# Kernel tuning notes

Hardware: AMD Instinct MI355X
Metric: run time of the kernel (lower is better)

The kernel has to match this reference:

```python
import jax, jax.numpy as jnp
import numpy as np

G = 160          # voxel grid extent per axis
N = 300000       # active voxels
CIN, COUT = 64, 128
EPS = 1e-4       # BatchNorm eps from module (0.0001)


def _neighbor_table(pos):
    """pos: [N,3] int32 in [0,G). Returns idx [27,N] int32, -1 where no neighbor voxel exists."""
    n = pos.shape[0]
    flat = (pos[:, 0] * G + pos[:, 1]) * G + pos[:, 2]
    grid = jnp.full((G * G * G,), -1, dtype=jnp.int32).at[flat].set(
        jnp.arange(n, dtype=jnp.int32))
    offs = jnp.array([[dx, dy, dz] for dx in (-1, 0, 1)
                      for dy in (-1, 0, 1) for dz in (-1, 0, 1)], dtype=jnp.int32)
    npos = pos[None, :, :] + offs[:, None, :]              # [27,N,3]
    inb = jnp.all((npos >= 0) & (npos < G), axis=-1)       # [27,N]
    nflat = (npos[..., 0] * G + npos[..., 1]) * G + npos[..., 2]
    nflat = jnp.where(inb, nflat, 0)
    return jnp.where(inb, grid[nflat], -1)                 # [27,N]


def _sparse_conv(feat, nbr_idx, W):
    """Submanifold sparse 3x3x3 conv. feat [N,Cin], nbr_idx [27,N], W [27,Cin,Cout]."""
    n = feat.shape[0]
    acc0 = jnp.zeros((n, W.shape[-1]), dtype=feat.dtype)

    def body(acc, xs):
        idx, Wk = xs                                       # [N], [Cin,Cout]
        valid = (idx >= 0)
        g = feat[jnp.maximum(idx, 0)] * valid[:, None].astype(feat.dtype)
        return acc + g @ Wk, None

    out, _ = jax.lax.scan(body, acc0, (nbr_idx, W))
    return out


def _bn(x, gamma, beta, mean, var):
    # eval-mode BatchNorm1d: (x - mean) / sqrt(var + eps) * gamma + beta
    return (x - mean) * jax.lax.rsqrt(var + EPS) * gamma + beta


def setup_inputs() -> dict:
    key = jax.random.key(0)
    ks = jax.random.split(key, 8)
    rng = np.random.default_rng(0)
    flat = rng.choice(G * G * G, size=N, replace=False)
    pos = np.stack(np.unravel_index(flat, (G, G, G)), axis=-1).astype(np.int32)

    feat = jax.random.normal(ks[0], (N, CIN), dtype=jnp.float32)
    lin_w = jax.random.normal(ks[1], (COUT, CIN), dtype=jnp.float32) / np.sqrt(CIN)
    W1 = jax.random.normal(ks[2], (27, CIN, COUT), dtype=jnp.float32) / np.sqrt(27 * CIN)
    W2 = jax.random.normal(ks[3], (27, COUT, COUT), dtype=jnp.float32) / np.sqrt(27 * COUT)
    return {
        "feat": feat,
        "pos": jnp.asarray(pos),
        "lin_w": lin_w,
        "bn1_gamma": jnp.ones((CIN,), jnp.float32),
        "bn1_beta": jnp.zeros((CIN,), jnp.float32),
        "bn1_mean": 0.1 * jax.random.normal(ks[4], (CIN,), dtype=jnp.float32),
        "bn1_var": 0.5 + jax.random.uniform(ks[5], (CIN,), dtype=jnp.float32),
        "W1": W1,
        "bn2_gamma": jnp.ones((COUT,), jnp.float32),
        "bn2_beta": jnp.zeros((COUT,), jnp.float32),
        "bn2_mean": 0.1 * jax.random.normal(ks[6], (COUT,), dtype=jnp.float32),
        "bn2_var": 0.5 + jax.random.uniform(ks[7], (COUT,), dtype=jnp.float32),
        "W2": W2,
    }


def reference(feat, pos, lin_w, bn1_gamma, bn1_beta, bn1_mean, bn1_var, W1,
              bn2_gamma, bn2_beta, bn2_mean, bn2_var, W2):
    nbr_idx = _neighbor_table(pos)                     # [27,N]
    out1 = feat @ lin_w.T                              # NetworkInNetwork skip
    h = jnp.maximum(_bn(feat, bn1_gamma, bn1_beta, bn1_mean, bn1_var), 0.0)  # LeakyReLU(0)==ReLU
    h = _sparse_conv(h, nbr_idx, W1)
    h = jnp.maximum(_bn(h, bn2_gamma, bn2_beta, bn2_mean, bn2_var), 0.0)
    h = _sparse_conv(h, nbr_idx, W2)
    return out1 + h
```

## Files before the change

kernel.cpp:

```cpp
#include <hip/hip_runtime.h>

#define G    160
#define G3   (G*G*G)
#define NV   300000
#define EPS  1e-4f
#define CAP  24576
#define CPAD 32

typedef unsigned short u16;
typedef __attribute__((ext_vector_type(8))) short bf16x8;
typedef __attribute__((ext_vector_type(4))) float f32x4;

#define OFF_PART 0ull
#define OFF_GRID 0ull
#define OFF_PIN  169869312ull
#define OFF_PSL  (OFF_PIN + 2654208ull)
#define OFF_CNT  (OFF_PSL + 19200000ull)
#define OFF_H0   (OFF_CNT + 4096ull)
#define OFF_H1   (OFF_H0  + 38400000ull)
#define OFF_W1T  (OFF_H1  + 76800000ull)
#define OFF_W2T  (OFF_W1T + 442368ull)
#define OFF_LINW (OFF_W2T + 884736ull)
#define OFF_BNP  (OFF_LINW + 16384ull)
#define WS_NEED  (OFF_BNP + 1024ull)

__device__ __forceinline__ u16 f2bf(float f) {
  unsigned u = __float_as_uint(f);
  return (u16)((u + 0x7fffu + ((u >> 16) & 1u)) >> 16);
}
__device__ __forceinline__ float bf2f(u16 h) {
  return __uint_as_float(((unsigned)h) << 16);
}

__global__ void k_grid(const int* __restrict__ pos, int* __restrict__ grid) {
  int i = blockIdx.x * 256 + threadIdx.x;
  if (i < NV)
    grid[(pos[3*i] * G + pos[3*i+1]) * G + pos[3*i+2]] = i;
}

__global__ __launch_bounds__(256) void k_pairs(const int* __restrict__ pos,
                        const int* __restrict__ grid,
                        int* __restrict__ pin, u16* __restrict__ pslot,
                        int* __restrict__ counts) {
  __shared__ int lcnt[27];
  __shared__ int wboff[27][4];
  __shared__ int gbase[27];
  int t = threadIdx.x, lane = t & 63, wv = t >> 6;
  if (t < 27) lcnt[t] = 0;
  int i = blockIdx.x * 256 + t;
  bool act = (i < NV);
  int p0 = 0, p1 = 1 << 20, p2 = 0;
  if (act) { p0 = pos[3*i]; p1 = pos[3*i+1]; p2 = pos[3*i+2]; }
  __syncthreads();

  int j[26];
  #pragma unroll
  for (int kk = 0; kk < 26; kk++) {
    int k = kk < 13 ? kk : kk + 1;
    int q0 = p0 + k/9 - 1, q1 = p1 + (k/3)%3 - 1, q2 = p2 + k%3 - 1;
    bool inb = (q0 >= 0 && q0 < G && q1 >= 0 && q1 < G && q2 >= 0 && q2 < G);
    int addr = inb ? (q0*G + q1)*G + q2 : 0;
    int jj = grid[addr];
    j[kk] = inb ? jj : -1;
  }

  unsigned long long m[26];
  #pragma unroll
  for (int kk = 0; kk < 26; kk++) m[kk] = __ballot(j[kk] >= 0);

  #pragma unroll
  for (int kk = 0; kk < 26; kk++) {
    int k = kk < 13 ? kk : kk + 1;
    if (lane == 0) wboff[k][wv] = atomicAdd(&lcnt[k], (int)__popcll(m[kk]));
  }
  __syncthreads();
  if (t < 27 && t != 13)
    gbase[t] = atomicAdd(&counts[t * CPAD], lcnt[t]);
  __syncthreads();

  #pragma unroll
  for (int kk = 0; kk < 26; kk++) {
    if (j[kk] >= 0) {
      int k = kk < 13 ? kk : kk + 1;
      int slot = gbase[k] + wboff[k][wv] + (int)__popcll(m[kk] & ((1ull << lane) - 1ull));
      if (slot < CAP) {
        pin[k*CAP + slot] = j[kk];
        pslot[(long)i*32 + k] = (u16)slot;
      }
    }
  }
}

__global__ void k_bn1(const float* __restrict__ feat, const float* g, const float* b,
                      const float* m, const float* v, u16* __restrict__ h0) {
  __shared__ float ss[64], tt[64];
  int t = threadIdx.x;
  if (t < 64) { float s = g[t] * rsqrtf(v[t] + EPS); ss[t] = s; tt[t] = b[t] - m[t]*s; }
  __syncthreads();
  long gt = (long)blockIdx.x * 256 + t;
  if (gt >= (long)NV * 16) return;
  int c = (int)(gt & 15) * 4;
  float4 x = ((const float4*)feat)[gt];
  ushort4 q;
  q.x = f2bf(fmaxf(x.x*ss[c  ] + tt[c  ], 0.f));
  q.y = f2bf(fmaxf(x.y*ss[c+1] + tt[c+1], 0.f));
  q.z = f2bf(fmaxf(x.z*ss[c+2] + tt[c+2], 0.f));
  q.w = f2bf(fmaxf(x.w*ss[c+3] + tt[c+3], 0.f));
  ((ushort4*)h0)[gt] = q;
}

__global__ void k_weights(const float* __restrict__ W1, const float* __restrict__ W2,
                          const float* __restrict__ linw,
                          const float* __restrict__ g2, const float* __restrict__ b2,
                          const float* __restrict__ m2, const float* __restrict__ v2,
                          u16* __restrict__ w1t, u16* __restrict__ w2t, u16* __restrict__ lwt,
                          float* __restrict__ bnp) {
  __shared__ float tmp[8192];
  int b = blockIdx.x, t = threadIdx.x;
  if (b < 27) {
    const float* src = W1 + b * 8192;
    u16* dst = w1t + b * 8192;
    for (int u = t; u < 8192; u += 256) tmp[u] = src[u];
    __syncthreads();
    for (int u = t; u < 8192; u += 256) { int c = u >> 6, a = u & 63; dst[c*64 + a] = f2bf(tmp[a*128 + c]); }
  } else if (b < 54) {
    int k = b - 27;
    const float* src = W2 + k * 16384;
    u16* dst = w2t + k * 16384;
    for (int h = 0; h < 2; h++) {
      for (int u = t; u < 8192; u += 256) tmp[u] = src[h*8192 + u];
      __syncthreads();
      for (int u = t; u < 8192; u += 256) { int c = u >> 6, a = u & 63; dst[c*128 + h*64 + a] = f2bf(tmp[a*128 + c]); }
      __syncthreads();
    }
  } else if (b == 54) {
    for (int u = t; u < 8192; u += 256) lwt[u] = f2bf(linw[u]);
  } else {
    if (t < 128) { float s = g2[t] * rsqrtf(v2[t] + EPS); bnp[t] = s; bnp[128 + t] = b2[t] - m2[t]*s; }
  }
}

template<int K, int RS>
__device__ __forceinline__ void stage_rows(const u16* __restrict__ src, const int* sidx, u16* lds) {
  const int LPR = K / 8, RPI = 256 / LPR;
  int t = threadIdx.x, o = t % LPR, r0 = t / LPR;
  #pragma unroll
  for (int r = r0; r < 128; r += RPI) {
    int j = sidx[r];
    int4 val = make_int4(0, 0, 0, 0);
    if (j >= 0) val = *(const int4*)(src + (long)j * RS + o * 8);
    *(int4*)(lds + r * (K + 8) + o * 8) = val;
  }
}

__device__ __forceinline__ void stage_feat(const float* __restrict__ feat, int row0, u16* lds) {
  int t = threadIdx.x, o = t & 15, r0 = t >> 4;
  #pragma unroll
  for (int r = r0; r < 128; r += 16) {
    int row = row0 + r;
    float4 x = make_float4(0.f, 0.f, 0.f, 0.f);
    if (row < NV) x = *(const float4*)(feat + (long)row * 64 + o * 4);
    ushort4 q; q.x = f2bf(x.x); q.y = f2bf(x.y); q.z = f2bf(x.z); q.w = f2bf(x.w);
    *(ushort4*)(lds + r * 72 + o * 4) = q;
  }
}

template<int K>
__device__ __forceinline__ void mma_tile(const u16* As, const u16* __restrict__ wt, f32x4 acc[4][4]) {
  int lane = threadIdx.x & 63, wave = threadIdx.x >> 6;
  int wr = (wave >> 1) * 64, wc = (wave & 1) * 64;
  int lr = lane & 15, lk = (lane >> 4) * 8;
  #pragma unroll
  for (int kk = 0; kk < K; kk += 32) {
    bf16x8 a[4], b[4];
    #pragma unroll
    for (int f = 0; f < 4; f++) a[f] = *(const bf16x8*)(As + (wr + f*16 + lr) * (K + 8) + kk + lk);
    #pragma unroll
    for (int f = 0; f < 4; f++) b[f] = *(const bf16x8*)(wt + (wc + f*16 + lr) * K + kk + lk);
    #pragma unroll
    for (int fr = 0; fr < 4; fr++)
      #pragma unroll
      for (int fc = 0; fc < 4; fc++)
        acc[fr][fc] = __builtin_amdgcn_mfma_f32_16x16x32_bf16(a[fr], b[fc], acc[fr][fc], 0, 0, 0);
  }
}

__device__ __forceinline__ void spill_acc(const f32x4 acc[4][4], u16* As) {
  int t = threadIdx.x, lane = t & 63, wave = t >> 6;
  int wr = (wave >> 1) * 64, wc = (wave & 1) * 64, cr = (lane >> 4) * 4, cc = lane & 15;
  #pragma unroll
  for (int fr = 0; fr < 4; fr++)
    #pragma unroll
    for (int r = 0; r < 4; r++)
      #pragma unroll
      for (int fc = 0; fc < 4; fc++)
        As[(wr + fr*16 + cr + r) * 136 + wc + fc*16 + cc] = f2bf(acc[fr][fc][r]);
}

template<int K, int RS>
__global__ __launch_bounds__(256, 4) void k_scat(const u16* __restrict__ h, const u16* __restrict__ wt,
                                                 const int* __restrict__ pin,
                                                 const int* __restrict__ counts,
                                                 u16* __restrict__ partial) {
  int k = blockIdx.y;
  int cnt = counts[k * CPAD]; if (cnt > CAP) cnt = CAP;
  int base = blockIdx.x * 128;
  if (base >= cnt) return;
  __shared__ __align__(16) u16 As[128 * 136];
  __shared__ int sin[128];
  int t = threadIdx.x;
  if (t < 128) sin[t] = (base + t < cnt) ? pin[k*CAP + base + t] : -1;
  __syncthreads();
  stage_rows<K, RS>(h, sin, As);
  __syncthreads();
  f32x4 acc[4][4] = {};
  mma_tile<K>(As, wt + k * (K * 128), acc);
  __syncthreads();
  spill_acc(acc, As);
  __syncthreads();
  #pragma unroll
  for (int u = t; u < 2048; u += 256) {
    int r = u >> 4, o = u & 15;
    if (base + r < cnt)
      *(int4*)(partial + ((long)k*CAP + base + r) * 128 + o * 8) = *(const int4*)(As + r * 136 + o * 8);
  }
}

__global__ __launch_bounds__(256, 4) void k_self1(const u16* __restrict__ h0,
                                                  const u16* __restrict__ w1t,
                                                  u16* __restrict__ h1) {
  __shared__ __align__(16) u16 As[128 * 136];
  __shared__ int sidx[128];
  int t = threadIdx.x, row0 = blockIdx.x * 128;
  if (t < 128) sidx[t] = (row0 + t < NV) ? row0 + t : -1;
  __syncthreads();
  stage_rows<64, 64>(h0, sidx, As);
  __syncthreads();
  f32x4 acc[4][4] = {};
  mma_tile<64>(As, w1t + 13 * 8192, acc);
  __syncthreads();
  spill_acc(acc, As);
  __syncthreads();
  #pragma unroll
  for (int u = t; u < 2048; u += 256) {
    int r = u >> 4, o = u & 15;
    if (row0 + r < NV)
      *(int4*)(h1 + (long)(row0 + r) * 128 + o * 8) = *(const int4*)(As + r * 136 + o * 8);
  }
}

__global__ __launch_bounds__(256, 4) void k_self2(const float* __restrict__ feat,
                                                  const u16* __restrict__ lwt,
                                                  u16* __restrict__ h1,
                                                  const u16* __restrict__ w2t) {
  __shared__ __align__(16) u16 As[128 * 136];
  __shared__ int sidx[128];
  int t = threadIdx.x, row0 = blockIdx.x * 128;
  if (t < 128) sidx[t] = (row0 + t < NV) ? row0 + t : -1;
  __syncthreads();
  f32x4 acc[4][4] = {};
  stage_feat(feat, row0, As);
  __syncthreads();
  mma_tile<64>(As, lwt, acc);
  __syncthreads();
  stage_rows<128, 128>(h1, sidx, As);
  __syncthreads();
  mma_tile<128>(As, w2t + 13 * 16384, acc);
  __syncthreads();
  spill_acc(acc, As);
  __syncthreads();
  #pragma unroll
  for (int u = t; u < 2048; u += 256) {
    int r = u >> 4, o = u & 15;
    if (row0 + r < NV)
      *(int4*)(h1 + (long)(row0 + r) * 128 + o * 8) = *(const int4*)(As + r * 136 + o * 8);
  }
}

__device__ __forceinline__ void gather_row(int row, int q,
                                           const u16* __restrict__ sp,
                                           const u16* __restrict__ pslot,
                                           const u16* __restrict__ partial,
                                           float c[32]) {
  int4 sv4[4];
  #pragma unroll
  for (int u = 0; u < 4; u++)
    sv4[u] = *(const int4*)((const char*)pslot + (long)row * 64 + u * 16);
  const u16* sv = (const u16*)sv4;
  bf16x8 s0[4];
  #pragma unroll
  for (int u = 0; u < 4; u++) s0[u] = *(const bf16x8*)(sp + (long)row * 128 + q * 32 + u * 8);
  #pragma unroll
  for (int u = 0; u < 4; u++)
    #pragma unroll
    for (int e = 0; e < 8; e++) c[u*8 + e] = bf2f((u16)s0[u][e]);
  #pragma unroll
  for (int k = 0; k < 27; k++) {
    if (k == 13) continue;
    unsigned s = sv[k];
    if (s < CAP) {
      const u16* pr = partial + ((long)k * CAP + s) * 128 + q * 32;
      bf16x8 pv[4];
      #pragma unroll
      for (int u = 0; u < 4; u++) pv[u] = *(const bf16x8*)(pr + u * 8);
      #pragma unroll
      for (int u = 0; u < 4; u++)
        #pragma unroll
        for (int e = 0; e < 8; e++) c[u*8 + e] += bf2f((u16)pv[u][e]);
    }
  }
}

__global__ __launch_bounds__(256, 4) void k_gather1(const u16* __restrict__ pslot,
                                                    const u16* __restrict__ partial,
                                                    const float* __restrict__ bnp,
                                                    u16* __restrict__ h1) {
  long tid = (long)blockIdx.x * 256 + threadIdx.x;
  int row = (int)(tid >> 2), q = (int)(tid & 3);
  if (row >= NV) return;
  float c[32];
  gather_row(row, q, h1, pslot, partial, c);
  int col0 = q * 32;
  unsigned w[16];
  #pragma unroll
  for (int e = 0; e < 16; e++) {
    float o0 = fmaxf(c[2*e  ] * bnp[col0 + 2*e  ] + bnp[128 + col0 + 2*e  ], 0.f);
    float o1 = fmaxf(c[2*e+1] * bnp[col0 + 2*e+1] + bnp[128 + col0 + 2*e+1], 0.f);
    w[e] = (unsigned)f2bf(o0) | ((unsigned)f2bf(o1) << 16);
  }
  int4* dst = (int4*)(h1 + (long)row * 128 + col0);
  #pragma unroll
  for (int u = 0; u < 4; u++) dst[u] = make_int4(w[4*u], w[4*u+1], w[4*u+2], w[4*u+3]);
}

__global__ __launch_bounds__(256, 4) void k_gather2(const u16* __restrict__ pslot,
                                                    const u16* __restrict__ partial,
                                                    const u16* __restrict__ h1,
                                                    float* __restrict__ out) {
  long tid = (long)blockIdx.x * 256 + threadIdx.x;
  int row = (int)(tid >> 2), q = (int)(tid & 3);
  if (row >= NV) return;
  float c[32];
  gather_row(row, q, h1, pslot, partial, c);
  float* dst = out + (long)row * 128 + q * 32;
  #pragma unroll
  for (int u = 0; u < 8; u++) {
    f32x4 v;
    #pragma unroll
    for (int e = 0; e < 4; e++) v[e] = c[u*4 + e];
    *(f32x4*)(dst + u * 4) = v;
  }
}

extern "C" void kernel_launch(void* const* d_in, const int* in_sizes, int n_in,
                              void* d_out, int out_size, void* d_ws, size_t ws_size,
                              hipStream_t stream) {
  const float* feat = (const float*)d_in[0];
  const int*   pos  = (const int*)d_in[1];
  const float* linw = (const float*)d_in[2];
  const float* g1 = (const float*)d_in[3], *b1 = (const float*)d_in[4];
  const float* m1 = (const float*)d_in[5], *v1 = (const float*)d_in[6];
  const float* W1 = (const float*)d_in[7];
  const float* g2 = (const float*)d_in[8], *b2 = (const float*)d_in[9];
  const float* m2 = (const float*)d_in[10], *v2 = (const float*)d_in[11];
  const float* W2 = (const float*)d_in[12];

  if (ws_size < WS_NEED) return;

  char* ws = (char*)d_ws;
  u16*   partial = (u16*)(ws + OFF_PART);
  int*   grid    = (int*)(ws + OFF_GRID);
  int*   pin     = (int*)(ws + OFF_PIN);
  u16*   pslot   = (u16*)(ws + OFF_PSL);
  int*   counts  = (int*)(ws + OFF_CNT);
  u16*   h0      = (u16*)(ws + OFF_H0);
  u16*   h1      = (u16*)(ws + OFF_H1);
  u16*   w1t     = (u16*)(ws + OFF_W1T);
  u16*   w2t     = (u16*)(ws + OFF_W2T);
  u16*   lwt     = (u16*)(ws + OFF_LINW);
  float* bnp     = (float*)(ws + OFF_BNP);
  float* out     = (float*)d_out;

  hipMemsetAsync(grid,  0xFF, (size_t)G3 * 4, stream);
  hipMemsetAsync(pslot, 0xFF, (size_t)NV * 32 * 2, stream);
  hipMemsetAsync(counts, 0, 27 * CPAD * 4, stream);

  k_grid  <<<(NV + 255) / 256, 256, 0, stream>>>(pos, grid);
  k_pairs <<<(NV + 255) / 256, 256, 0, stream>>>(pos, grid, pin, pslot, counts);
  k_bn1   <<<(NV * 16) / 256, 256, 0, stream>>>(feat, g1, b1, m1, v1, h0);
  k_weights<<<56, 256, 0, stream>>>(W1, W2, linw, g2, b2, m2, v2, w1t, w2t, lwt, bnp);

  dim3 gt((NV + 127) / 128);
  dim3 gscat(CAP / 128, 27);
  dim3 gg(((long)NV * 4 + 255) / 256);
  k_scat<64, 64>   <<<gscat, 256, 0, stream>>>(h0, w1t, pin, counts, partial);
  k_self1          <<<gt, 256, 0, stream>>>(h0, w1t, h1);
  k_gather1        <<<gg, 256, 0, stream>>>(pslot, partial, bnp, h1);
  k_scat<128, 128> <<<gscat, 256, 0, stream>>>(h1, w2t, pin, counts, partial);
  k_self2          <<<gt, 256, 0, stream>>>(feat, lwt, h1, w2t);
  k_gather2        <<<gg, 256, 0, stream>>>(pslot, partial, h1, out);
}
```

Baseline: 782.4 us.

## Write scatter partials in per-row CSR order so gathers read contiguously

The pair-building kernel now prefix-scans each voxel's neighbor count and assigns it a contiguous block of partial-product slots, storing a packed base/count per row. The scatter GEMM writes each result row directly into that CSR position instead of a per-offset array. The gather kernels then stream the row's partials sequentially without reading a 27-entry slot table, and the 19 MB pslot memset is dropped. The cost is a block-level scan with extra barriers in k_pairs and scattered, uncoalesced row writes in k_scat.

New measurement: 676.8 us. 13.5% less time.

```diff
diff --git a/kernel.cpp b/kernel.cpp
--- a/kernel.cpp
+++ b/kernel.cpp
@@ -6,6 +6,8 @@
 #define EPS  1e-4f
 #define CAP  24576
 #define CPAD 32
+#define PCAP 655360
+#define TOTIDX 896
 
 typedef unsigned short u16;
 typedef __attribute__((ext_vector_type(8))) short bf16x8;
@@ -13,16 +15,17 @@
 
 #define OFF_PART 0ull
 #define OFF_GRID 0ull
-#define OFF_PIN  169869312ull
-#define OFF_PSL  (OFF_PIN + 2654208ull)
-#define OFF_CNT  (OFF_PSL + 19200000ull)
-#define OFF_H0   (OFF_CNT + 4096ull)
-#define OFF_H1   (OFF_H0  + 38400000ull)
-#define OFF_W1T  (OFF_H1  + 76800000ull)
-#define OFF_W2T  (OFF_W1T + 442368ull)
-#define OFF_LINW (OFF_W2T + 884736ull)
+#define OFF_PIN  167772160ull
+#define OFF_PDST (OFF_PIN  + 2654208ull)
+#define OFF_RI   (OFF_PDST + 2654208ull)
+#define OFF_CNT  (OFF_RI   + 1200000ull)
+#define OFF_H0   (OFF_CNT  + 4096ull)
+#define OFF_H1   (OFF_H0   + 38400000ull)
+#define OFF_W1T  (OFF_H1   + 76800000ull)
+#define OFF_W2T  (OFF_W1T  + 442368ull)
+#define OFF_LINW (OFF_W2T  + 884736ull)
 #define OFF_BNP  (OFF_LINW + 16384ull)
-#define WS_NEED  (OFF_BNP + 1024ull)
+#define WS_NEED  (OFF_BNP  + 1024ull)
 
 __device__ __forceinline__ u16 f2bf(float f) {
   unsigned u = __float_as_uint(f);
@@ -40,11 +43,13 @@
 
 __global__ __launch_bounds__(256) void k_pairs(const int* __restrict__ pos,
                         const int* __restrict__ grid,
-                        int* __restrict__ pin, u16* __restrict__ pslot,
-                        int* __restrict__ counts) {
+                        int* __restrict__ pin, int* __restrict__ pdst,
+                        int* __restrict__ rowinfo, int* __restrict__ counts) {
   __shared__ int lcnt[27];
   __shared__ int wboff[27][4];
   __shared__ int gbase[27];
+  __shared__ int scan[256];
+  __shared__ int sgb;
   int t = threadIdx.x, lane = t & 63, wv = t >> 6;
   if (t < 27) lcnt[t] = 0;
   int i = blockIdx.x * 256 + t;
@@ -64,6 +69,11 @@
     j[kk] = inb ? jj : -1;
   }
 
+  unsigned vmask = 0;
+  #pragma unroll
+  for (int kk = 0; kk < 26; kk++) if (j[kk] >= 0) vmask |= 1u << kk;
+  int ci = __popc(vmask);
+
   unsigned long long m[26];
   #pragma unroll
   for (int kk = 0; kk < 26; kk++) m[kk] = __ballot(j[kk] >= 0);
@@ -73,19 +83,33 @@
     int k = kk < 13 ? kk : kk + 1;
     if (lane == 0) wboff[k][wv] = atomicAdd(&lcnt[k], (int)__popcll(m[kk]));
   }
-  __syncthreads();
+  scan[t] = ci;
+  __syncthreads();
+  #pragma unroll
+  for (int d = 1; d < 256; d <<= 1) {
+    int val = (t >= d) ? scan[t - d] : 0;
+    __syncthreads();
+    scan[t] += val;
+    __syncthreads();
+  }
   if (t < 27 && t != 13)
     gbase[t] = atomicAdd(&counts[t * CPAD], lcnt[t]);
-  __syncthreads();
+  if (t == 255) sgb = atomicAdd(&counts[TOTIDX], scan[255]);
+  __syncthreads();
+
+  int rbase = sgb + scan[t] - ci;
+  int cw = (rbase + ci > PCAP) ? 0 : ci;
+  if (act) rowinfo[i] = (rbase << 5) | cw;
 
   #pragma unroll
   for (int kk = 0; kk < 26; kk++) {
     if (j[kk] >= 0) {
       int k = kk < 13 ? kk : kk + 1;
       int slot = gbase[k] + wboff[k][wv] + (int)__popcll(m[kk] & ((1ull << lane) - 1ull));
+      int dst = rbase + __popc(vmask & ((1u << kk) - 1u));
       if (slot < CAP) {
-        pin[k*CAP + slot] = j[kk];
-        pslot[(long)i*32 + k] = (u16)slot;
+        pin[k*CAP + slot]  = j[kk];
+        pdst[k*CAP + slot] = (dst < PCAP) ? dst : -1;
       }
     }
   }
@@ -200,6 +224,7 @@
 template<int K, int RS>
 __global__ __launch_bounds__(256, 4) void k_scat(const u16* __restrict__ h, const u16* __restrict__ wt,
                                                  const int* __restrict__ pin,
+                                                 const int* __restrict__ pdst,
                                                  const int* __restrict__ counts,
                                                  u16* __restrict__ partial) {
   int k = blockIdx.y;
@@ -207,9 +232,10 @@
   int base = blockIdx.x * 128;
   if (base >= cnt) return;
   __shared__ __align__(16) u16 As[128 * 136];
-  __shared__ int sin[128];
+  __shared__ int sin[128], sdst[128];
   int t = threadIdx.x;
   if (t < 128) sin[t] = (base + t < cnt) ? pin[k*CAP + base + t] : -1;
+  else         sdst[t - 128] = (base + t - 128 < cnt) ? pdst[k*CAP + base + t - 128] : -1;
   __syncthreads();
   stage_rows<K, RS>(h, sin, As);
   __syncthreads();
@@ -221,8 +247,9 @@
   #pragma unroll
   for (int u = t; u < 2048; u += 256) {
     int r = u >> 4, o = u & 15;
-    if (base + r < cnt)
-      *(int4*)(partial + ((long)k*CAP + base + r) * 128 + o * 8) = *(const int4*)(As + r * 136 + o * 8);
+    int d = sdst[r];
+    if (d >= 0)
+      *(int4*)(partial + (long)d * 128 + o * 8) = *(const int4*)(As + r * 136 + o * 8);
   }
 }
 
@@ -277,49 +304,54 @@
   }
 }
 
-__device__ __forceinline__ void gather_row(int row, int q,
+__device__ __forceinline__ void gather_csr(int row, int q, int base, int cnt,
                                            const u16* __restrict__ sp,
-                                           const u16* __restrict__ pslot,
                                            const u16* __restrict__ partial,
                                            float c[32]) {
-  int4 sv4[4];
+  bf16x8 s0[4];
+  const u16* srow = sp + (long)row * 128 + q * 32;
+  #pragma unroll
+  for (int u = 0; u < 4; u++) s0[u] = *(const bf16x8*)(srow + u * 8);
   #pragma unroll
   for (int u = 0; u < 4; u++)
-    sv4[u] = *(const int4*)((const char*)pslot + (long)row * 64 + u * 16);
-  const u16* sv = (const u16*)sv4;
-  bf16x8 s0[4];
-  #pragma unroll
-  for (int u = 0; u < 4; u++) s0[u] = *(const bf16x8*)(sp + (long)row * 128 + q * 32 + u * 8);
-  #pragma unroll
-  for (int u = 0; u < 4; u++)
     #pragma unroll
     for (int e = 0; e < 8; e++) c[u*8 + e] = bf2f((u16)s0[u][e]);
-  #pragma unroll
-  for (int k = 0; k < 27; k++) {
-    if (k == 13) continue;
-    unsigned s = sv[k];
-    if (s < CAP) {
-      const u16* pr = partial + ((long)k * CAP + s) * 128 + q * 32;
-      bf16x8 pv[4];
+  const u16* pr = partial + (long)base * 128 + q * 32;
+  int p = 0;
+  for (; p + 2 <= cnt; p += 2) {
+    bf16x8 a[4], b[4];
+    #pragma unroll
+    for (int u = 0; u < 4; u++) a[u] = *(const bf16x8*)(pr + u * 8);
+    #pragma unroll
+    for (int u = 0; u < 4; u++) b[u] = *(const bf16x8*)(pr + 128 + u * 8);
+    #pragma unroll
+    for (int u = 0; u < 4; u++)
       #pragma unroll
-      for (int u = 0; u < 4; u++) pv[u] = *(const bf16x8*)(pr + u * 8);
+      for (int e = 0; e < 8; e++) c[u*8 + e] += bf2f((u16)a[u][e]) + bf2f((u16)b[u][e]);
+    pr += 256;
+  }
+  if (p < cnt) {
+    bf16x8 a[4];
+    #pragma unroll
+    for (int u = 0; u < 4; u++) a[u] = *(const bf16x8*)(pr + u * 8);
+    #pragma unroll
+    for (int u = 0; u < 4; u++)
       #pragma unroll
-      for (int u = 0; u < 4; u++)
-        #pragma unroll
-        for (int e = 0; e < 8; e++) c[u*8 + e] += bf2f((u16)pv[u][e]);
-    }
-  }
-}
-
-__global__ __launch_bounds__(256, 4) void k_gather1(const u16* __restrict__ pslot,
-                                                    const u16* __restrict__ partial,
-                                                    const float* __restrict__ bnp,
-                                                    u16* __restrict__ h1) {
+      for (int e = 0; e < 8; e++) c[u*8 + e] += bf2f((u16)a[u][e]);
+  }
+}
+
+__global__ __launch_bounds__(256) void k_gather1(const int* __restrict__ rowinfo,
+                                                 const u16* __restrict__ partial,
+                                                 const float* __restrict__ bnp,
+                                                 u16* __restrict__ h1) {
   long tid = (long)blockIdx.x * 256 + threadIdx.x;
   int row = (int)(tid >> 2), q = (int)(tid & 3);
   if (row >= NV) return;
+  int ri = rowinfo[row];
+  int base = (int)((unsigned)ri >> 5), cnt = ri & 31;
   float c[32];
-  gather_row(row, q, h1, pslot, partial, c);
+  gather_csr(row, q, base, cnt, h1, partial, c);
   int col0 = q * 32;
   unsigned w[16];
   #pragma unroll
@@ -333,15 +365,17 @@
   for (int u = 0; u < 4; u++) dst[u] = make_int4(w[4*u], w[4*u+1], w[4*u+2], w[4*u+3]);
 }
 
-__global__ __launch_bounds__(256, 4) void k_gather2(const u16* __restrict__ pslot,
-                                                    const u16* __restrict__ partial,
-                                                    const u16* __restrict__ h1,
-                                                    float* __restrict__ out) {
+__global__ __launch_bounds__(256) void k_gather2(const int* __restrict__ rowinfo,
+                                                 const u16* __restrict__ partial,
+                                                 const u16* __restrict__ h1,
+                                                 float* __restrict__ out) {
   long tid = (long)blockIdx.x * 256 + threadIdx.x;
   int row = (int)(tid >> 2), q = (int)(tid & 3);
   if (row >= NV) return;
+  int ri = rowinfo[row];
+  int base = (int)((unsigned)ri >> 5), cnt = ri & 31;
   float c[32];
-  gather_row(row, q, h1, pslot, partial, c);
+  gather_csr(row, q, base, cnt, h1, partial, c);
   float* dst = out + (long)row * 128 + q * 32;
   #pragma unroll
   for (int u = 0; u < 8; u++) {
@@ -371,7 +405,8 @@
   u16*   partial = (u16*)(ws + OFF_PART);
   int*   grid    = (int*)(ws + OFF_GRID);
   int*   pin     = (int*)(ws + OFF_PIN);
-  u16*   pslot   = (u16*)(ws + OFF_PSL);
+  int*   pdst    = (int*)(ws + OFF_PDST);
+  int*   rowinfo = (int*)(ws + OFF_RI);
   int*   counts  = (int*)(ws + OFF_CNT);
   u16*   h0      = (u16*)(ws + OFF_H0);
   u16*   h1      = (u16*)(ws + OFF_H1);
@@ -382,21 +417,20 @@
   float* out     = (float*)d_out;
 
   hipMemsetAsync(grid,  0xFF, (size_t)G3 * 4, stream);
-  hipMemsetAsync(pslot, 0xFF, (size_t)NV * 32 * 2, stream);
-  hipMemsetAsync(counts, 0, 27 * CPAD * 4, stream);
+  hipMemsetAsync(counts, 0, 4096, stream);
 
   k_grid  <<<(NV + 255) / 256, 256, 0, stream>>>(pos, grid);
-  k_pairs <<<(NV + 255) / 256, 256, 0, stream>>>(pos, grid, pin, pslot, counts);
+  k_pairs <<<(NV + 255) / 256, 256, 0, stream>>>(pos, grid, pin, pdst, rowinfo, counts);
   k_bn1   <<<(NV * 16) / 256, 256, 0, stream>>>(feat, g1, b1, m1, v1, h0);
   k_weights<<<56, 256, 0, stream>>>(W1, W2, linw, g2, b2, m2, v2, w1t, w2t, lwt, bnp);
 
   dim3 gt((NV + 127) / 128);
   dim3 gscat(CAP / 128, 27);
   dim3 gg(((long)NV * 4 + 255) / 256);
-  k_scat<64, 64>   <<<gscat, 256, 0, stream>>>(h0, w1t, pin, counts, partial);
+  k_scat<64, 64>   <<<gscat, 256, 0, stream>>>(h0, w1t, pin, pdst, counts, partial);
   k_self1          <<<gt, 256, 0, stream>>>(h0, w1t, h1);
-  k_gather1        <<<gg, 256, 0, stream>>>(pslot, partial, bnp, h1);
-  k_scat<128, 128> <<<gscat, 256, 0, stream>>>(h1, w2t, pin, counts, partial);
+  k_gather1        <<<gg, 256, 0, stream>>>(rowinfo, partial, bnp, h1);
+  k_scat<128, 128> <<<gscat, 256, 0, stream>>>(h1, w2t, pin, pdst, counts, partial);
   k_self2          <<<gt, 256, 0, stream>>>(feat, lwt, h1, w2t);
-  k_gather2        <<<gg, 256, 0, stream>>>(pslot, partial, h1, out);
-}
+  k_gather2        <<<gg, 256, 0, stream>>>(rowinfo, partial, h1, out);
+}
```
